# Performance work log

Measured on AMD Instinct MI355X. Metric: run time of the kernel, lower is better.

## Reference

```python
import jax, jax.numpy as jnp
import numpy as np


def setup_inputs() -> dict:
    key = jax.random.key(0)
    k1, k2 = jax.random.split(key)
    B, N, D = 4, 4096, 512
    q = jax.random.normal(k1, (B, N, D), dtype=jnp.float32)
    kv = jax.random.normal(k2, (B, N, D), dtype=jnp.float32)
    return {"q": q, "kv": kv}


def reference(q, kv):
    # q, kv: [B, N, D]
    scale = (kv.shape[-1] // 2) ** (-0.5)
    # full QK^T needed for the softmax row normalizer: [B, N, N]
    scores = jnp.einsum('bnd,bmd->bnm', q, kv) * scale
    lse = jax.nn.logsumexp(scores, axis=-1)          # [B, N]
    # diagonal logits computed directly (avoids re-reading the full matrix)
    diag = jnp.einsum('bnd,bnd->bn', q, kv) * scale  # [B, N]
    # masked_select with an eye mask returns the diagonal softmax entries,
    # flattened in row-major order -> shape [B*N]
    return jnp.exp(diag - lse).reshape(-1)
```

## Files before the change

kernel.cpp:

```cpp
#include <hip/hip_runtime.h>
#include <hip/hip_fp16.h>


typedef _Float16 f16x8 __attribute__((ext_vector_type(8)));
typedef float    f32x4 __attribute__((ext_vector_type(4)));

#define NB 4
#define NN 4096
#define ND 512
#define SCALE 0.0625f
#define LOG2E 1.4426950408889634f
#define NROWS (NB * NN)
#define FRAG_B 1024
#define GRP_B  16384
#define TILE_B 32768
#define CPITCH 520

__device__ __forceinline__ void gld16(const void* g, void* l) {
    __builtin_amdgcn_global_load_lds(
        (const __attribute__((address_space(1))) unsigned int*)g,
        (__attribute__((address_space(3))) unsigned int*)l, 16, 0, 0);
}

__device__ __forceinline__ f16x8 cvt8(float4 a, float4 b) {
    f16x8 r;
    r[0] = (_Float16)a.x; r[1] = (_Float16)a.y; r[2] = (_Float16)a.z; r[3] = (_Float16)a.w;
    r[4] = (_Float16)b.x; r[5] = (_Float16)b.y; r[6] = (_Float16)b.z; r[7] = (_Float16)b.w;
    return r;
}

__device__ __forceinline__ f16x8 cvt8s(float4 a, float4 b, float s) {
    f16x8 r;
    r[0] = (_Float16)(a.x * s); r[1] = (_Float16)(a.y * s);
    r[2] = (_Float16)(a.z * s); r[3] = (_Float16)(a.w * s);
    r[4] = (_Float16)(b.x * s); r[5] = (_Float16)(b.y * s);
    r[6] = (_Float16)(b.z * s); r[7] = (_Float16)(b.w * s);
    return r;
}

__launch_bounds__(256)
__global__ void convert_kernel(const float* __restrict__ kv,
                               _Float16* __restrict__ kvp) {
    __shared__ _Float16 s[16 * CPITCH];
    const int g    = blockIdx.x;
    const int tid  = threadIdx.x;
    const int wid  = tid >> 6;
    const int lane = tid & 63;
    const int l15  = lane & 15;
    const int quad = lane >> 4;

    #pragma unroll
    for (int i = 0; i < 4; ++i) {
        const int r = wid * 4 + i;
        const float* src = kv + ((size_t)g * 16 + r) * ND + lane * 8;
        float4 a = *(const float4*)src;
        float4 b = *(const float4*)(src + 4);
        *(f16x8*)(s + r * CPITCH + lane * 8) = cvt8(a, b);
    }
    __syncthreads();

    _Float16* dst = kvp + (size_t)g * 8192 + lane * 8;
    #pragma unroll
    for (int p = 0; p < 4; ++p) {
        const int kt = wid * 4 + p;
        f16x8 v = *(const f16x8*)(s + l15 * CPITCH + kt * 32 + quad * 8);
        *(f16x8*)(dst + kt * 512) = v;
    }
}

__launch_bounds__(256, 2)
__global__ void lse_partial_kernel(const float* __restrict__ q,
                                   const _Float16* __restrict__ kvp,
                                   float* __restrict__ partial,
                                   float* __restrict__ diagsc) {
    __shared__ char sbuf[2][TILE_B];

    const int bc = blockIdx.x;
    const int b  = bc >> 2;
    const int cs = bc & 3;
    const int rb = blockIdx.y;
    const int tid  = threadIdx.x;
    const int wid  = tid >> 6;
    const int lane = tid & 63;
    const int l15  = lane & 15;
    const int quad = lane >> 4;

    const int row0 = rb * 128 + wid * 32;
    const int it_diag = ((row0 >> 10) == cs) ? ((row0 - cs * 1024) >> 5) : -1;

    f16x8 Af[2][16];
    #pragma unroll
    for (int m = 0; m < 2; ++m) {
        const float* qrow = q + ((size_t)(b * NN + row0 + m * 16 + l15)) * ND + quad * 8;
        #pragma unroll
        for (int k = 0; k < 16; ++k) {
            float4 u0 = *(const float4*)(qrow + k * 32);
            float4 u1 = *(const float4*)(qrow + k * 32 + 4);
            Af[m][k] = cvt8s(u0, u1, SCALE * LOG2E);
        }
    }

    float lacc[2][4];
    #pragma unroll
    for (int m = 0; m < 2; ++m)
        #pragma unroll
        for (int j = 0; j < 4; ++j)
            lacc[m][j] = 0.f;

    const char* pb  = (const char*)kvp + ((size_t)(b * 256 + cs * 64)) * GRP_B;
    const char* ssb = pb + (size_t)lane * 16;

    #define STAGE(it_, buf_)                                                  \
        do {                                                                  \
            const char* sp_ = ssb + (size_t)(it_) * TILE_B;                   \
            char* lb_ = sbuf[buf_];                                           \
            _Pragma("unroll")                                                 \
            for (int p_ = 0; p_ < 8; ++p_) {                                  \
                int f_ = wid * 8 + p_;                                        \
                gld16(sp_ + f_ * FRAG_B, lb_ + f_ * FRAG_B);                  \
            }                                                                 \
        } while (0)

    STAGE(0, 0);
    int buf = 0;

    for (int it = 0; it < 32; ++it) {
        __syncthreads();
        if (it + 1 < 32) STAGE(it + 1, buf ^ 1);

        const char* lb = sbuf[buf] + (size_t)lane * 16;
        f32x4 acc[2][2];
        #pragma unroll
        for (int m = 0; m < 2; ++m)
            #pragma unroll
            for (int nf = 0; nf < 2; ++nf)
                acc[m][nf] = (f32x4){0.f, 0.f, 0.f, 0.f};

        #pragma unroll
        for (int kt = 0; kt < 16; ++kt) {
            f16x8 b0 = *(const f16x8*)(lb + kt * FRAG_B);
            f16x8 b1 = *(const f16x8*)(lb + GRP_B + kt * FRAG_B);
            acc[0][0] = __builtin_amdgcn_mfma_f32_16x16x32_f16(Af[0][kt], b0, acc[0][0], 0, 0, 0);
            acc[1][0] = __builtin_amdgcn_mfma_f32_16x16x32_f16(Af[1][kt], b0, acc[1][0], 0, 0, 0);
            acc[0][1] = __builtin_amdgcn_mfma_f32_16x16x32_f16(Af[0][kt], b1, acc[0][1], 0, 0, 0);
            acc[1][1] = __builtin_amdgcn_mfma_f32_16x16x32_f16(Af[1][kt], b1, acc[1][1], 0, 0, 0);
        }

        if (it == it_diag) {
            if ((l15 >> 2) == quad) {
                const int j = l15 & 3;
                float d0 = (j == 0) ? acc[0][0][0] : (j == 1) ? acc[0][0][1]
                         : (j == 2) ? acc[0][0][2] : acc[0][0][3];
                float d1 = (j == 0) ? acc[1][1][0] : (j == 1) ? acc[1][1][1]
                         : (j == 2) ? acc[1][1][2] : acc[1][1][3];
                diagsc[b * NN + row0 + l15]      = d0;
                diagsc[b * NN + row0 + 16 + l15] = d1;
            }
        }

        #pragma unroll
        for (int m = 0; m < 2; ++m)
            #pragma unroll
            for (int nf = 0; nf < 2; ++nf)
                #pragma unroll
                for (int j = 0; j < 4; ++j)
                    lacc[m][j] += __builtin_amdgcn_exp2f(acc[m][nf][j]);

        buf ^= 1;
    }

    #pragma unroll
    for (int m = 0; m < 2; ++m)
        #pragma unroll
        for (int j = 0; j < 4; ++j) {
            float v = lacc[m][j];
            v += __shfl_xor(v, 1, 64);
            v += __shfl_xor(v, 2, 64);
            v += __shfl_xor(v, 4, 64);
            v += __shfl_xor(v, 8, 64);
            if (l15 == 0)
                partial[(size_t)cs * NROWS + b * NN + row0 + m * 16 + quad * 4 + j] = v;
        }
}

__launch_bounds__(256)
__global__ void finalize_kernel(const float* __restrict__ partial,
                                const float* __restrict__ diagsc,
                                float* __restrict__ out) {
    const int idx = blockIdx.x * 256 + threadIdx.x;
    float l = partial[idx] + partial[NROWS + idx] +
              partial[2 * NROWS + idx] + partial[3 * NROWS + idx];
    out[idx] = exp2f(diagsc[idx]) / l;
}

extern "C" void kernel_launch(void* const* d_in, const int* in_sizes, int n_in,
                              void* d_out, int out_size, void* d_ws, size_t ws_size,
                              hipStream_t stream) {
    const float* q  = (const float*)d_in[0];
    const float* kv = (const float*)d_in[1];
    float* out = (float*)d_out;

    _Float16* kvp   = (_Float16*)d_ws;
    float* partial  = (float*)((char*)d_ws + (size_t)NROWS * ND * 2);
    float* diagsc   = partial + 4 * NROWS;

    convert_kernel<<<1024, 256, 0, stream>>>(kv, kvp);
    lse_partial_kernel<<<dim3(16, 32), 256, 0, stream>>>(q, kvp, partial, diagsc);
    finalize_kernel<<<NROWS / 256, 256, 0, stream>>>(partial, diagsc, out);
}
```

Baseline: 162.4 us.

## Overlap first KV tile load with Q load and software-pipeline LDS fragment reads

The first global-to-LDS stage of KV is issued before the Q fragments are loaded and converted, so the two fetches overlap. The main loop swaps __syncthreads for an explicit vmcnt(0) wait plus s_barrier and ping-pongs two buffer pointers. LDS B-fragment reads are double-buffered two k-steps ahead of the MFMAs, and wave priority is raised around the MFMA block. This adds register pressure and relies on the hand-written waitcnt being correct for the async LDS loads.

```diff
diff --git a/kernel.cpp b/kernel.cpp
--- a/kernel.cpp
+++ b/kernel.cpp
@@ -11,10 +11,12 @@
 #define SCALE 0.0625f
 #define LOG2E 1.4426950408889634f
 #define NROWS (NB * NN)
+#define NCS 4
 #define FRAG_B 1024
 #define GRP_B  16384
 #define TILE_B 32768
 #define CPITCH 520
+#define NIT 32
 
 __device__ __forceinline__ void gld16(const void* g, void* l) {
     __builtin_amdgcn_global_load_lds(
@@ -88,6 +90,24 @@
     const int row0 = rb * 128 + wid * 32;
     const int it_diag = ((row0 >> 10) == cs) ? ((row0 - cs * 1024) >> 5) : -1;
 
+    const char* pb  = (const char*)kvp + ((size_t)(b * 256 + cs * 64)) * GRP_B;
+    const char* ssb = pb + (size_t)lane * 16;
+
+    char* cur = sbuf[0];
+    char* nxt = sbuf[1];
+
+    #define STAGE(it_, dst_)                                                  \
+        do {                                                                  \
+            const char* sp_ = ssb + (size_t)(it_) * TILE_B;                   \
+            _Pragma("unroll")                                                 \
+            for (int p_ = 0; p_ < 8; ++p_) {                                  \
+                int f_ = wid * 8 + p_;                                        \
+                gld16(sp_ + (size_t)f_ * FRAG_B, (dst_) + (size_t)f_ * FRAG_B); \
+            }                                                                 \
+        } while (0)
+
+    STAGE(0, cur);
+
     f16x8 Af[2][16];
     #pragma unroll
     for (int m = 0; m < 2; ++m) {
@@ -107,28 +127,7 @@
         for (int j = 0; j < 4; ++j)
             lacc[m][j] = 0.f;
 
-    const char* pb  = (const char*)kvp + ((size_t)(b * 256 + cs * 64)) * GRP_B;
-    const char* ssb = pb + (size_t)lane * 16;
-
-    #define STAGE(it_, buf_)                                                  \
-        do {                                                                  \
-            const char* sp_ = ssb + (size_t)(it_) * TILE_B;                   \
-            char* lb_ = sbuf[buf_];                                           \
-            _Pragma("unroll")                                                 \
-            for (int p_ = 0; p_ < 8; ++p_) {                                  \
-                int f_ = wid * 8 + p_;                                        \
-                gld16(sp_ + f_ * FRAG_B, lb_ + f_ * FRAG_B);                  \
-            }                                                                 \
-        } while (0)
-
-    STAGE(0, 0);
-    int buf = 0;
-
-    for (int it = 0; it < 32; ++it) {
-        __syncthreads();
-        if (it + 1 < 32) STAGE(it + 1, buf ^ 1);
-
-        const char* lb = sbuf[buf] + (size_t)lane * 16;
+    for (int it = 0; it < NIT; ++it) {
         f32x4 acc[2][2];
         #pragma unroll
         for (int m = 0; m < 2; ++m)
@@ -136,15 +135,43 @@
             for (int nf = 0; nf < 2; ++nf)
                 acc[m][nf] = (f32x4){0.f, 0.f, 0.f, 0.f};
 
-        #pragma unroll
-        for (int kt = 0; kt < 16; ++kt) {
-            f16x8 b0 = *(const f16x8*)(lb + kt * FRAG_B);
-            f16x8 b1 = *(const f16x8*)(lb + GRP_B + kt * FRAG_B);
-            acc[0][0] = __builtin_amdgcn_mfma_f32_16x16x32_f16(Af[0][kt], b0, acc[0][0], 0, 0, 0);
-            acc[1][0] = __builtin_amdgcn_mfma_f32_16x16x32_f16(Af[1][kt], b0, acc[1][0], 0, 0, 0);
-            acc[0][1] = __builtin_amdgcn_mfma_f32_16x16x32_f16(Af[0][kt], b1, acc[0][1], 0, 0, 0);
-            acc[1][1] = __builtin_amdgcn_mfma_f32_16x16x32_f16(Af[1][kt], b1, acc[1][1], 0, 0, 0);
-        }
+        asm volatile("s_waitcnt vmcnt(0)" ::: "memory");
+        __builtin_amdgcn_s_barrier();
+        asm volatile("" ::: "memory");
+        if (it + 1 < NIT) STAGE(it + 1, nxt);
+
+        const char* lb = cur + (size_t)lane * 16;
+
+        f16x8 pb0[2], pb1[2];
+        pb0[0] = *(const f16x8*)(lb + 0 * FRAG_B);
+        pb1[0] = *(const f16x8*)(lb + GRP_B + 0 * FRAG_B);
+        pb0[1] = *(const f16x8*)(lb + 1 * FRAG_B);
+        pb1[1] = *(const f16x8*)(lb + GRP_B + 1 * FRAG_B);
+
+        __builtin_amdgcn_s_setprio(1);
+        #define KSTEP(kt_)                                                     \
+            do {                                                               \
+                acc[0][0] = __builtin_amdgcn_mfma_f32_16x16x32_f16(            \
+                    Af[0][kt_], pb0[(kt_) & 1], acc[0][0], 0, 0, 0);           \
+                acc[1][0] = __builtin_amdgcn_mfma_f32_16x16x32_f16(            \
+                    Af[1][kt_], pb0[(kt_) & 1], acc[1][0], 0, 0, 0);           \
+                acc[0][1] = __builtin_amdgcn_mfma_f32_16x16x32_f16(            \
+                    Af[0][kt_], pb1[(kt_) & 1], acc[0][1], 0, 0, 0);           \
+                acc[1][1] = __builtin_amdgcn_mfma_f32_16x16x32_f16(            \
+                    Af[1][kt_], pb1[(kt_) & 1], acc[1][1], 0, 0, 0);           \
+                if ((kt_) + 2 < 16) {                                          \
+                    pb0[(kt_) & 1] =                                           \
+                        *(const f16x8*)(lb + ((kt_) + 2) * FRAG_B);            \
+                    pb1[(kt_) & 1] =                                           \
+                        *(const f16x8*)(lb + GRP_B + ((kt_) + 2) * FRAG_B);    \
+                }                                                              \
+            } while (0)
+        KSTEP(0);  KSTEP(1);  KSTEP(2);  KSTEP(3);
+        KSTEP(4);  KSTEP(5);  KSTEP(6);  KSTEP(7);
+        KSTEP(8);  KSTEP(9);  KSTEP(10); KSTEP(11);
+        KSTEP(12); KSTEP(13); KSTEP(14); KSTEP(15);
+        #undef KSTEP
+        __builtin_amdgcn_s_setprio(0);
 
         if (it == it_diag) {
             if ((l15 >> 2) == quad) {
@@ -166,7 +193,7 @@
                 for (int j = 0; j < 4; ++j)
                     lacc[m][j] += __builtin_amdgcn_exp2f(acc[m][nf][j]);
 
-        buf ^= 1;
+        char* t = cur; cur = nxt; nxt = t;
     }
 
     #pragma unroll
@@ -188,8 +215,10 @@
                                 const float* __restrict__ diagsc,
                                 float* __restrict__ out) {
     const int idx = blockIdx.x * 256 + threadIdx.x;
-    float l = partial[idx] + partial[NROWS + idx] +
-              partial[2 * NROWS + idx] + partial[3 * NROWS + idx];
+    float l = 0.f;
+    #pragma unroll
+    for (int c = 0; c < NCS; ++c)
+        l += partial[(size_t)c * NROWS + idx];
     out[idx] = exp2f(diagsc[idx]) / l;
 }
 
@@ -202,7 +231,7 @@
 
     _Float16* kvp   = (_Float16*)d_ws;
     float* partial  = (float*)((char*)d_ws + (size_t)NROWS * ND * 2);
-    float* diagsc   = partial + 4 * NROWS;
+    float* diagsc   = partial + NCS * NROWS;
 
     convert_kernel<<<1024, 256, 0, stream>>>(kv, kvp);
     lse_partial_kernel<<<dim3(16, 32), 256, 0, stream>>>(q, kvp, partial, diagsc);
```

Result: no change. 162.3 us (-0.1%).
